# Kernel tuning notes

Hardware: AMD Instinct MI355X
Metric: run time of the kernel (lower is better)

The kernel has to match this reference:

```python
import jax, jax.numpy as jnp
import numpy as np

G = 1        # num_dispatch_groups
C = 8        # dispatch_group_size (chips)
EPC = 4      # experts_per_chip
E = 32       # num_routed_experts
K = 8        # num_experts_per_tok
S = 256      # seq_len_per_chip
H = 2048     # hidden_dim
M = 2048     # max_dispatched_tokens_per_expert
ML = 8       # metadata_len
CAP = M // C # per-chip slot region per expert
# expert_dispatch_table: expert e lives on chip e // EPC (all present)
TABLE = jnp.asarray(np.arange(E) // EPC, dtype=jnp.int32)[None, :]  # (G, E)


def setup_inputs() -> dict:
    key = jax.random.key(0)
    k1, k2, k3 = jax.random.split(key, 3)
    x = jax.random.normal(k1, (C, S, H), dtype=jnp.float32)
    weights = jax.random.uniform(k2, (C, S, K), dtype=jnp.float32)
    indices = jax.random.randint(k3, (C, S, K), 0, E).astype(jnp.int32)
    # each source chip writes into its own disjoint slot region per expert
    expert_offsets = jnp.broadcast_to((jnp.arange(C, dtype=jnp.int32) * CAP)[:, None], (C, E))
    return {"x": x, "weights": weights, "indices": indices, "expert_offsets": expert_offsets}


def _dst_slots(indices, expert_offsets):
    """Replicates the sequential offset_copy bookkeeping: dst = base offset +
    number of earlier (token, topk) picks of the same expert on the same chip."""
    idx = indices.reshape(C, S * K)  # flat (token, topk) order matches loop order
    oh = (idx[:, :, None] == jnp.arange(E, dtype=jnp.int32)[None, None, :]).astype(jnp.int32)  # [C, SK, E]
    rank = jnp.take_along_axis(jnp.cumsum(oh, axis=1) - oh, idx[..., None], axis=2)[..., 0]    # [C, SK]
    base = jnp.take_along_axis(expert_offsets, idx, axis=1)                                     # [C, SK]
    return idx, base + rank


def reference(x, weights, indices, expert_offsets):
    idx, dst = _dst_slots(indices, expert_offsets)                 # [C, SK]
    tokens = jnp.arange(S * K, dtype=jnp.int32) // K               # token id per flat pos
    topk = jnp.arange(S * K, dtype=jnp.int32) % K                  # topk id per flat pos
    vals = x[:, tokens]                                            # [C, SK, H] gather
    # bf16 weight bits viewed as int16, sign-extended into int32 (matches torch .view(int16))
    wbits = jax.lax.bitcast_convert_type(weights.astype(jnp.bfloat16), jnp.int16).astype(jnp.int32).reshape(C, S * K)
    chips = jnp.broadcast_to(jnp.arange(C, dtype=jnp.int32)[:, None], (C, S * K))
    meta_rows = jnp.stack(
        [chips, jnp.broadcast_to(tokens, (C, S * K)), jnp.broadcast_to(topk, (C, S * K)), idx, wbits]
        + [jnp.zeros((C, S * K), jnp.int32)] * (ML - 5), axis=-1)  # [C, SK, ML]
    eic = idx % EPC                                                # expert index within chip

    buf = jnp.zeros((G, C, EPC, M, H), dtype=jnp.float32)
    meta = jnp.full((G, C, EPC, M, ML), -1, dtype=jnp.int32)
    for g in range(G):
        ec = TABLE[g][idx]                                         # destination chip per dispatch
        ec = jnp.where(ec >= 0, ec, C)                             # -1 -> out of bounds -> dropped
        f = lambda a: a.reshape(-1)
        buf = buf.at[g, f(ec), f(eic), f(dst)].set(vals.reshape(-1, H), mode='drop')
        meta = meta.at[g, f(ec), f(eic), f(dst)].set(meta_rows.reshape(-1, ML), mode='drop')
    return buf, meta
```

## Files before the change

kernel.cpp:

```cpp
#include <hip/hip_runtime.h>
#include <hip/hip_bf16.h>
#include <stdint.h>

#define C_   8
#define EPC_ 4
#define E_   32
#define K_   8
#define S_   256
#define H_   2048
#define M_   2048
#define ML_  8
#define CAP_ 256
#define SK_  2048
#define NROWS_ (E_ * M_)
#define BUF_ELEMS_ ((size_t)E_ * M_ * H_)
#define ROWS_PER_BLOCK_ 4

typedef float f32x4 __attribute__((ext_vector_type(4)));

__global__ __launch_bounds__(64) void rank_kernel(
        const int* __restrict__ indices,
        const int* __restrict__ expert_offsets,
        int* __restrict__ inv,
        int* __restrict__ cnt) {
    const int c    = blockIdx.x >> 5;
    const int e    = blockIdx.x & 31;
    const int lane = threadIdx.x;
    const int* __restrict__ ip = indices + c * SK_;
    const int base = expert_offsets[c * E_ + e];

    int running = 0;
    const unsigned long long below = (lane == 63) ? ~0ULL >> 1
                                                  : (1ULL << lane) - 1ULL;
    #pragma unroll 4
    for (int ch = 0; ch < SK_ / 64; ++ch) {
        const int i = ch * 64 + lane;
        const bool hit = (ip[i] == e);
        const unsigned long long m = __ballot(hit);
        if (hit) {
            const int rank = running + __popcll(m & below);
            const int dst  = base + rank;
            if ((unsigned)dst < (unsigned)M_) {
                inv[e * M_ + dst] = c * SK_ + i;
            }
        }
        running += __popcll(m);
    }
    if (lane == 0) cnt[c * E_ + e] = running;
}

__global__ __launch_bounds__(256) void fill_rows(
        const float* __restrict__ x,
        const float* __restrict__ w,
        const int* __restrict__ inv,
        const int* __restrict__ cnt,
        float* __restrict__ buf,
        float* __restrict__ meta) {
    const int r0 = blockIdx.x * ROWS_PER_BLOCK_;
    const int t  = threadIdx.x;

    int cn[ROWS_PER_BLOCK_], iv[ROWS_PER_BLOCK_];
    #pragma unroll
    for (int j = 0; j < ROWS_PER_BLOCK_; ++j) {
        const int r    = r0 + j;
        const int e    = r >> 11;
        const int dst  = r & (M_ - 1);
        const int c    = dst >> 8;
        cn[j] = cnt[c * E_ + e];
        iv[j] = inv[r];
    }
    int p[ROWS_PER_BLOCK_];
    #pragma unroll
    for (int j = 0; j < ROWS_PER_BLOCK_; ++j) {
        const int slot = (r0 + j) & (CAP_ - 1);
        p[j] = (slot < cn[j]) ? iv[j] : -1;
    }

    const f32x4 z = {0.f, 0.f, 0.f, 0.f};
    #pragma unroll
    for (int j = 0; j < ROWS_PER_BLOCK_; ++j) {
        const int r = r0 + j;
        f32x4* __restrict__ brow = reinterpret_cast<f32x4*>(buf + (size_t)r * H_);
        if (p[j] < 0) {
            __builtin_nontemporal_store(z, brow + t);
            __builtin_nontemporal_store(z, brow + t + 256);
        } else {
            const int pp    = p[j];
            const int c     = pp >> 11;
            const int i     = pp & (SK_ - 1);
            const int token = i >> 3;
            const f32x4* __restrict__ src =
                reinterpret_cast<const f32x4*>(x + ((size_t)(c * S_ + token)) * H_);
            const f32x4 a = src[t];
            const f32x4 b = src[t + 256];
            __builtin_nontemporal_store(a, brow + t);
            __builtin_nontemporal_store(b, brow + t + 256);
        }
    }

    if (t < ROWS_PER_BLOCK_) {
        const int j  = t;
        const int r  = r0 + j;
        const int pp = p[j];
        f32x4* __restrict__ mrow = reinterpret_cast<f32x4*>(meta + (size_t)r * ML_);
        if (pp < 0) {
            const f32x4 m = {-1.f, -1.f, -1.f, -1.f};
            __builtin_nontemporal_store(m, mrow);
            __builtin_nontemporal_store(m, mrow + 1);
        } else {
            const int c     = pp >> 11;
            const int i     = pp & (SK_ - 1);
            const int token = i >> 3;
            const int topk  = i & (K_ - 1);
            const int e     = r >> 11;
            const float wv    = w[pp];
            const uint32_t u  = __float_as_uint(wv);
            const uint32_t rb = (u + 0x7FFFu + ((u >> 16) & 1u)) >> 16;
            const int wb      = (int)(short)(unsigned short)rb;
            const f32x4 m0 = {(float)c, (float)token, (float)topk, (float)e};
            const f32x4 m1 = {(float)wb, 0.f, 0.f, 0.f};
            __builtin_nontemporal_store(m0, mrow);
            __builtin_nontemporal_store(m1, mrow + 1);
        }
    }
}

extern "C" void kernel_launch(void* const* d_in, const int* in_sizes, int n_in,
                              void* d_out, int out_size, void* d_ws, size_t ws_size,
                              hipStream_t stream) {
    const float* x   = (const float*)d_in[0];
    const float* w   = (const float*)d_in[1];
    const int* idx   = (const int*)d_in[2];
    const int* eo    = (const int*)d_in[3];

    float* buf  = (float*)d_out;
    float* meta = buf + BUF_ELEMS_;

    int* inv = (int*)d_ws;
    int* cnt = inv + NROWS_;

    rank_kernel<<<C_ * E_, 64, 0, stream>>>(idx, eo, inv, cnt);
    fill_rows<<<NROWS_ / ROWS_PER_BLOCK_, 256, 0, stream>>>(x, w, inv, cnt, buf, meta);
}
```

Measured before the change: 115.6 us.

## Switch to source-driven scatter with separate zero-fill kernel

Each block now reads one source token row once and scatters it to up to K destination rows. Before, each destination row gathered its own source row, so the same x row was read up to K times. A separate kernel zero-fills only the unoccupied slots and writes -1 metadata for them, using per-chip expert counts. This adds a third kernel launch and makes the writes scattered rather than sequential. The output is still written exactly once per row.

```diff
diff --git a/kernel.cpp b/kernel.cpp
--- a/kernel.cpp
+++ b/kernel.cpp
@@ -14,14 +14,14 @@
 #define SK_  2048
 #define NROWS_ (E_ * M_)
 #define BUF_ELEMS_ ((size_t)E_ * M_ * H_)
-#define ROWS_PER_BLOCK_ 4
+#define ZROWS_PER_BLOCK_ 4
 
 typedef float f32x4 __attribute__((ext_vector_type(4)));
 
 __global__ __launch_bounds__(64) void rank_kernel(
         const int* __restrict__ indices,
         const int* __restrict__ expert_offsets,
-        int* __restrict__ inv,
+        int* __restrict__ dstmap,
         int* __restrict__ cnt) {
     const int c    = blockIdx.x >> 5;
     const int e    = blockIdx.x & 31;
@@ -30,7 +30,7 @@
     const int base = expert_offsets[c * E_ + e];
 
     int running = 0;
-    const unsigned long long below = (lane == 63) ? ~0ULL >> 1
+    const unsigned long long below = (lane == 63) ? (~0ULL >> 1)
                                                   : (1ULL << lane) - 1ULL;
     #pragma unroll 4
     for (int ch = 0; ch < SK_ / 64; ++ch) {
@@ -38,90 +38,88 @@
         const bool hit = (ip[i] == e);
         const unsigned long long m = __ballot(hit);
         if (hit) {
-            const int rank = running + __popcll(m & below);
-            const int dst  = base + rank;
-            if ((unsigned)dst < (unsigned)M_) {
-                inv[e * M_ + dst] = c * SK_ + i;
-            }
+            const int dst = base + running + __popcll(m & below);
+            dstmap[c * SK_ + i] =
+                ((unsigned)dst < (unsigned)M_) ? (e * M_ + dst) : -1;
         }
         running += __popcll(m);
     }
     if (lane == 0) cnt[c * E_ + e] = running;
 }
 
-__global__ __launch_bounds__(256) void fill_rows(
+__global__ __launch_bounds__(256) void gather_fill(
         const float* __restrict__ x,
         const float* __restrict__ w,
-        const int* __restrict__ inv,
-        const int* __restrict__ cnt,
+        const int* __restrict__ dstmap,
         float* __restrict__ buf,
         float* __restrict__ meta) {
-    const int r0 = blockIdx.x * ROWS_PER_BLOCK_;
-    const int t  = threadIdx.x;
+    const int b     = blockIdx.x;
+    const int c     = b >> 8;
+    const int token = b & (S_ - 1);
+    const int t     = threadIdx.x;
 
-    int cn[ROWS_PER_BLOCK_], iv[ROWS_PER_BLOCK_];
+    const f32x4* __restrict__ src = reinterpret_cast<const f32x4*>(x + (size_t)b * H_);
+    const f32x4 a0 = src[t];
+    const f32x4 a1 = src[t + 256];
+
+    const int* __restrict__ dm = dstmap + c * SK_ + token * K_;
+    int d[K_];
     #pragma unroll
-    for (int j = 0; j < ROWS_PER_BLOCK_; ++j) {
-        const int r    = r0 + j;
-        const int e    = r >> 11;
-        const int dst  = r & (M_ - 1);
-        const int c    = dst >> 8;
-        cn[j] = cnt[c * E_ + e];
-        iv[j] = inv[r];
-    }
-    int p[ROWS_PER_BLOCK_];
+    for (int k = 0; k < K_; ++k) d[k] = dm[k];
+
     #pragma unroll
-    for (int j = 0; j < ROWS_PER_BLOCK_; ++j) {
-        const int slot = (r0 + j) & (CAP_ - 1);
-        p[j] = (slot < cn[j]) ? iv[j] : -1;
-    }
-
-    const f32x4 z = {0.f, 0.f, 0.f, 0.f};
-    #pragma unroll
-    for (int j = 0; j < ROWS_PER_BLOCK_; ++j) {
-        const int r = r0 + j;
-        f32x4* __restrict__ brow = reinterpret_cast<f32x4*>(buf + (size_t)r * H_);
-        if (p[j] < 0) {
-            __builtin_nontemporal_store(z, brow + t);
-            __builtin_nontemporal_store(z, brow + t + 256);
-        } else {
-            const int pp    = p[j];
-            const int c     = pp >> 11;
-            const int i     = pp & (SK_ - 1);
-            const int token = i >> 3;
-            const f32x4* __restrict__ src =
-                reinterpret_cast<const f32x4*>(x + ((size_t)(c * S_ + token)) * H_);
-            const f32x4 a = src[t];
-            const f32x4 b = src[t + 256];
-            __builtin_nontemporal_store(a, brow + t);
-            __builtin_nontemporal_store(b, brow + t + 256);
+    for (int k = 0; k < K_; ++k) {
+        if (d[k] >= 0) {
+            f32x4* __restrict__ brow = reinterpret_cast<f32x4*>(buf + (size_t)d[k] * H_);
+            __builtin_nontemporal_store(a0, brow + t);
+            __builtin_nontemporal_store(a1, brow + t + 256);
         }
     }
 
-    if (t < ROWS_PER_BLOCK_) {
-        const int j  = t;
-        const int r  = r0 + j;
-        const int pp = p[j];
-        f32x4* __restrict__ mrow = reinterpret_cast<f32x4*>(meta + (size_t)r * ML_);
-        if (pp < 0) {
-            const f32x4 m = {-1.f, -1.f, -1.f, -1.f};
-            __builtin_nontemporal_store(m, mrow);
-            __builtin_nontemporal_store(m, mrow + 1);
-        } else {
-            const int c     = pp >> 11;
-            const int i     = pp & (SK_ - 1);
-            const int token = i >> 3;
-            const int topk  = i & (K_ - 1);
-            const int e     = r >> 11;
-            const float wv    = w[pp];
+    if (t < K_) {
+        const int k  = t;
+        const int dd = d[k];
+        if (dd >= 0) {
+            const int e = dd >> 11;
+            const float wv    = w[b * K_ + k];
             const uint32_t u  = __float_as_uint(wv);
             const uint32_t rb = (u + 0x7FFFu + ((u >> 16) & 1u)) >> 16;
             const int wb      = (int)(short)(unsigned short)rb;
-            const f32x4 m0 = {(float)c, (float)token, (float)topk, (float)e};
+            f32x4* __restrict__ mrow = reinterpret_cast<f32x4*>(meta + (size_t)dd * ML_);
+            const f32x4 m0 = {(float)c, (float)token, (float)k, (float)e};
             const f32x4 m1 = {(float)wb, 0.f, 0.f, 0.f};
             __builtin_nontemporal_store(m0, mrow);
             __builtin_nontemporal_store(m1, mrow + 1);
         }
+    }
+}
+
+__global__ __launch_bounds__(256) void zero_fill(
+        const int* __restrict__ cnt,
+        float* __restrict__ buf,
+        float* __restrict__ meta) {
+    const int r0    = blockIdx.x * ZROWS_PER_BLOCK_;
+    const int e     = r0 >> 11;
+    const int dst0  = r0 & (M_ - 1);
+    const int c     = dst0 >> 8;
+    const int slot0 = dst0 & (CAP_ - 1);
+
+    int nocc = cnt[c * E_ + e] - slot0;
+    if (nocc >= ZROWS_PER_BLOCK_) return;
+    if (nocc < 0) nocc = 0;
+
+    const int t = threadIdx.x;
+    const f32x4 z = {0.f, 0.f, 0.f, 0.f};
+    for (int j = nocc; j < ZROWS_PER_BLOCK_; ++j) {
+        f32x4* __restrict__ brow = reinterpret_cast<f32x4*>(buf + (size_t)(r0 + j) * H_);
+        __builtin_nontemporal_store(z, brow + t);
+        __builtin_nontemporal_store(z, brow + t + 256);
+    }
+    if (t >= nocc && t < ZROWS_PER_BLOCK_) {
+        f32x4* __restrict__ mrow = reinterpret_cast<f32x4*>(meta + (size_t)(r0 + t) * ML_);
+        const f32x4 m = {-1.f, -1.f, -1.f, -1.f};
+        __builtin_nontemporal_store(m, mrow);
+        __builtin_nontemporal_store(m, mrow + 1);
     }
 }
 
@@ -136,9 +134,10 @@
     float* buf  = (float*)d_out;
     float* meta = buf + BUF_ELEMS_;
 
-    int* inv = (int*)d_ws;
-    int* cnt = inv + NROWS_;
+    int* dstmap = (int*)d_ws;
+    int* cnt    = dstmap + C_ * SK_;
 
-    rank_kernel<<<C_ * E_, 64, 0, stream>>>(idx, eo, inv, cnt);
-    fill_rows<<<NROWS_ / ROWS_PER_BLOCK_, 256, 0, stream>>>(x, w, inv, cnt, buf, meta);
+    rank_kernel<<<C_ * E_, 64, 0, stream>>>(idx, eo, dstmap, cnt);
+    gather_fill<<<C_ * S_, 256, 0, stream>>>(x, w, dstmap, buf, meta);
+    zero_fill<<<NROWS_ / ZROWS_PER_BLOCK_, 256, 0, stream>>>(cnt, buf, meta);
 }
```

Measured after the change: 110.0 us. 1.05x faster.
